# Kernel tuning notes

Hardware: AMD Instinct MI355X
Metric: run time of the kernel (lower is better)

Reference implementation:

```python
import jax, jax.numpy as jnp
import numpy as np

T = 1024
HID = 2048
N_HEADS = 32
N_KV = 8
HEAD_DIM = HID // N_HEADS  # 64
Q_SIZE = N_HEADS * HEAD_DIM
KV_SIZE = N_KV * HEAD_DIM
N_EXP = 32
TOP_K = 4
FF = 1792
EPS = 1e-5
THETA = 1e6
SCALE = HEAD_DIM ** -0.5
ROUTED_SCALE = 1.0
CAP = 2 * (T * TOP_K // N_EXP)


def rmsnorm(x, w, eps=EPS):
    xf = x.astype(jnp.float32)
    var = jnp.mean(xf * xf, axis=-1, keepdims=True)
    return ((xf * jax.lax.rsqrt(var + eps)).astype(x.dtype)) * w


def apply_rope(x, positions):
    # neox-style rotary, full head_dim. x: [T, h, D]
    half = x.shape[-1] // 2
    inv_freq = 1.0 / (THETA ** (jnp.arange(0, half, dtype=jnp.float32) / half))
    ang = positions.astype(jnp.float32)[:, None] * inv_freq  # [T, half]
    cos = jnp.cos(ang)[:, None, :]
    sin = jnp.sin(ang)[:, None, :]
    x1, x2 = x[..., :half], x[..., half:]
    return jnp.concatenate([x1 * cos - x2 * sin, x2 * cos + x1 * sin], axis=-1)


def setup_inputs() -> dict:
    key = jax.random.key(0)
    ks = jax.random.split(key, 12)
    s = 0.02
    return {
        "positions": jnp.arange(T, dtype=jnp.int32),
        "hidden_states": jax.random.normal(ks[0], (T, HID), jnp.float32),
        "residual": jax.random.normal(ks[1], (T, HID), jnp.float32),
        "w_qkv": jax.random.normal(ks[2], (HID, Q_SIZE + 2 * KV_SIZE), jnp.float32) * s,
        "w_out": jax.random.normal(ks[3], (HID, HID), jnp.float32) * s,
        "q_ln_w": 1.0 + jax.random.normal(ks[4], (HEAD_DIM,), jnp.float32) * s,
        "k_ln_w": 1.0 + jax.random.normal(ks[5], (HEAD_DIM,), jnp.float32) * s,
        "op_norm_w": 1.0 + jax.random.normal(ks[6], (HID,), jnp.float32) * s,
        "ffn_norm_w": 1.0 + jax.random.normal(ks[7], (HID,), jnp.float32) * s,
        "gate_w": jax.random.normal(ks[8], (HID, N_EXP), jnp.float32) * s,
        "gate_bias": jax.random.normal(ks[9], (N_EXP,), jnp.float32) * s,
        "w1": jax.random.normal(ks[10], (N_EXP, HID, 2 * FF), jnp.float32) * s,
        "w2": jax.random.normal(ks[11], (N_EXP, FF, HID), jnp.float32) * s,
    }


def moe_block(x, gate_w, gate_bias, w1, w2):
    # router: sigmoid scoring + correction bias for selection, weights from raw scores
    logits = (x @ gate_w).astype(jnp.float32)          # [T, E]
    scores = jax.nn.sigmoid(logits)
    _, topk_idx = jax.lax.top_k(scores + gate_bias, TOP_K)   # [T, K]
    tw = jnp.take_along_axis(scores, topk_idx, axis=-1)      # [T, K]
    tw = tw / jnp.sum(tw, axis=-1, keepdims=True)            # renormalize

    TK = T * TOP_K
    flat_e = topk_idx.reshape(-1)                      # [TK]
    flat_w = tw.reshape(-1)
    tok = jnp.repeat(jnp.arange(T), TOP_K)             # source token per pair
    order = jnp.argsort(flat_e)                        # stable group-by-expert
    se, sw, st = flat_e[order], flat_w[order], tok[order]
    counts = jnp.bincount(flat_e, length=N_EXP)
    offs = jnp.concatenate([jnp.zeros((1,), counts.dtype), jnp.cumsum(counts)[:-1]])
    pos = jnp.arange(TK) - offs[se]                    # slot within expert
    valid = (pos < CAP).astype(x.dtype)
    pos_c = jnp.minimum(pos, CAP - 1)

    # dispatch -> [E, CAP, H]
    buf = jnp.zeros((N_EXP, CAP, HID), x.dtype).at[se, pos_c].add(x[st] * valid[:, None])
    gu = jnp.einsum('ech,ehf->ecf', buf, w1)           # [E, CAP, 2F]
    g, u = gu[..., :FF], gu[..., FF:]
    h = jax.nn.silu(g) * u
    eo = jnp.einsum('ecf,efh->ech', h, w2)             # [E, CAP, H]

    # combine (gather + weighted scatter-add back to tokens)
    y_pairs = eo[se, pos_c] * (sw * valid)[:, None]
    out = jnp.zeros((T, HID), x.dtype).at[st].add(y_pairs)
    return out * ROUTED_SCALE


def reference(positions, hidden_states, residual, w_qkv, w_out, q_ln_w, k_ln_w,
              op_norm_w, ffn_norm_w, gate_w, gate_bias, w1, w2):
    # operator_norm with fused residual add
    x = hidden_states + residual
    res = x
    h = rmsnorm(x, op_norm_w)

    # attention
    qkv = h @ w_qkv
    q = qkv[:, :Q_SIZE].reshape(T, N_HEADS, HEAD_DIM)
    k = qkv[:, Q_SIZE:Q_SIZE + KV_SIZE].reshape(T, N_KV, HEAD_DIM)
    v = qkv[:, Q_SIZE + KV_SIZE:].reshape(T, N_KV, HEAD_DIM)
    q = rmsnorm(q, q_ln_w)
    k = rmsnorm(k, k_ln_w)
    q = apply_rope(q, positions)
    k = apply_rope(k, positions)
    rep = N_HEADS // N_KV
    kr = jnp.repeat(k, rep, axis=1)                    # [T, H, D]
    vr = jnp.repeat(v, rep, axis=1)
    scores = jnp.einsum('qhd,khd->hqk', q, kr) * SCALE
    causal = jnp.tril(jnp.ones((T, T), bool))
    scores = jnp.where(causal, scores, jnp.finfo(jnp.float32).min)
    p = jax.nn.softmax(scores.astype(jnp.float32), axis=-1).astype(h.dtype)
    a = jnp.einsum('hqk,khd->qhd', p, vr).reshape(T, HID)
    attn_out = a @ w_out

    # ffn_norm with fused residual add
    x2 = attn_out + res
    res2 = x2
    h2 = rmsnorm(x2, ffn_norm_w)

    out = moe_block(h2, gate_w, gate_bias, w1, w2)
    return out, res2
```

## Files before the change

### kernel.cpp

```cpp
#include <hip/hip_runtime.h>
#include <stdint.h>
#include <math.h>

typedef unsigned short ushort_t;
typedef __attribute__((ext_vector_type(8))) short short8;
typedef __attribute__((ext_vector_type(4))) float f32x4;

#define T_ 1024
#define HID_ 2048
#define NH_ 32
#define NKV_ 8
#define HD_ 64
#define QS_ 2048
#define KVS_ 512
#define QKVN_ 3072
#define NEXP_ 32
#define TOPK_ 4
#define FF_ 1792
#define FF2_ 3584
#define CAP_ 256
#define EPS_ 1e-5f
#define ATT_SCALE_ 0.125f

__device__ __forceinline__ ushort_t f2bf(float f) {
    uint32_t u = __builtin_bit_cast(uint32_t, f);
    u += 0x7FFFu + ((u >> 16) & 1u);
    return (ushort_t)(u >> 16);
}

__device__ __forceinline__ float bf2f(ushort_t u) {
    uint32_t x = ((uint32_t)u) << 16;
    return __builtin_bit_cast(float, x);
}

__device__ __forceinline__ f32x4 mfma16(short8 a, short8 b, f32x4 c) {
    return __builtin_amdgcn_mfma_f32_16x16x32_bf16(a, b, c, 0, 0, 0);
}

__device__ __forceinline__ uint32_t cvtpk(float lo, float hi) {
    uint32_t r;
    asm("v_cvt_pk_bf16_f32 %0, %1, %2" : "=v"(r) : "v"(lo), "v"(hi));
    return r;
}

__global__ __launch_bounds__(256) void k_addnorm(
    const float* __restrict__ a, const float* __restrict__ b,
    const float* __restrict__ w, float* __restrict__ res_out,
    float* __restrict__ hf, ushort_t* __restrict__ hb)
{
    __shared__ float sred[4];
    const int t = blockIdx.x;
    float x[8];
    float ss = 0.f;
#pragma unroll
    for (int i = 0; i < 8; i++) {
        int c = threadIdx.x + i * 256;
        float v = a[(size_t)t * HID_ + c];
        if (b) v += b[(size_t)t * HID_ + c];
        x[i] = v;
        ss += v * v;
    }
    ss += __shfl_xor(ss, 1);  ss += __shfl_xor(ss, 2);  ss += __shfl_xor(ss, 4);
    ss += __shfl_xor(ss, 8);  ss += __shfl_xor(ss, 16); ss += __shfl_xor(ss, 32);
    const int lane = threadIdx.x & 63, wv = threadIdx.x >> 6;
    if (lane == 0) sred[wv] = ss;
    __syncthreads();
    ss = sred[0] + sred[1] + sred[2] + sred[3];
    const float scale = rsqrtf(ss * (1.0f / HID_) + EPS_);
#pragma unroll
    for (int i = 0; i < 8; i++) {
        int c = threadIdx.x + i * 256;
        if (res_out) res_out[(size_t)t * HID_ + c] = x[i];
        float hv = x[i] * scale * w[c];
        if (hf) hf[(size_t)t * HID_ + c] = hv;
        hb[(size_t)t * HID_ + c] = f2bf(hv);
    }
}

__global__ __launch_bounds__(256) void k_rope_table(const int* __restrict__ positions,
                                                    float* __restrict__ cosb, float* __restrict__ sinb)
{
    int idx = blockIdx.x * 256 + threadIdx.x;
    if (idx >= T_ * 32) return;
    int t = idx >> 5, f = idx & 31;
    double invf = pow(1.0e6, -((double)f) / 32.0);
    double ang = (double)positions[t] * invf;
    cosb[idx] = (float)cos(ang);
    sinb[idx] = (float)sin(ang);
}

__global__ __launch_bounds__(256) void k_qkv_post(
    const float* __restrict__ qkv, const float* __restrict__ qw, const float* __restrict__ kw,
    const float* __restrict__ cosb, const float* __restrict__ sinb,
    ushort_t* __restrict__ qr, ushort_t* __restrict__ kc, ushort_t* __restrict__ vT)
{
    const int t = blockIdx.x;
    const int wv = threadIdx.x >> 6, lane = threadIdx.x & 63;
    const float* row = qkv + (size_t)t * QKVN_;
    const float c = cosb[t * 32 + (lane & 31)];
    const float s = sinb[t * 32 + (lane & 31)];
#pragma unroll
    for (int i = 0; i < 8; i++) {
        int hh = wv + i * 4;
        float x = row[hh * 64 + lane];
        float ss = x * x;
        ss += __shfl_xor(ss, 1); ss += __shfl_xor(ss, 2); ss += __shfl_xor(ss, 4);
        ss += __shfl_xor(ss, 8); ss += __shfl_xor(ss, 16); ss += __shfl_xor(ss, 32);
        float xn = x * rsqrtf(ss * (1.0f / 64.0f) + EPS_) * qw[lane];
        float other = __shfl_xor(xn, 32);
        float o = (lane < 32) ? (xn * c - other * s) : (xn * c + other * s);
        qr[(size_t)t * QS_ + hh * 64 + lane] = f2bf(o);
    }
#pragma unroll
    for (int i = 0; i < 2; i++) {
        int kh = wv * 2 + i;
        float x = row[QS_ + kh * 64 + lane];
        float ss = x * x;
        ss += __shfl_xor(ss, 1); ss += __shfl_xor(ss, 2); ss += __shfl_xor(ss, 4);
        ss += __shfl_xor(ss, 8); ss += __shfl_xor(ss, 16); ss += __shfl_xor(ss, 32);
        float xn = x * rsqrtf(ss * (1.0f / 64.0f) + EPS_) * kw[lane];
        float other = __shfl_xor(xn, 32);
        float o = (lane < 32) ? (xn * c - other * s) : (xn * c + other * s);
        kc[((size_t)kh * T_ + t) * 64 + lane] = f2bf(o);
    }
#pragma unroll
    for (int i = 0; i < 2; i++) {
        int idx = threadIdx.x + i * 256;
        int kh = idx >> 6, d = idx & 63;
        vT[((size_t)kh * 64 + d) * T_ + t] = f2bf(row[QS_ + KVS_ + idx]);
    }
}

__global__ __launch_bounds__(256) void k_attn(
    const ushort_t* __restrict__ qr, const ushort_t* __restrict__ kc,
    const ushort_t* __restrict__ vT, ushort_t* __restrict__ aout)
{
    __shared__ float p_lds[4][16][36];
    const int head = blockIdx.y;
    const int qb = blockIdx.x * 64;
    const int wv = threadIdx.x >> 6, lane = threadIdx.x & 63;
    const int lr = lane & 15, lg = lane >> 4;
    const int kvh = head >> 2;
    const int qbase = qb + wv * 16;

    const ushort_t* qp = qr + (size_t)(qbase + lr) * QS_ + head * 64 + lg * 8;
    short8 qf0 = *(const short8*)qp;
    short8 qf1 = *(const short8*)(qp + 32);

    f32x4 o[4];
#pragma unroll
    for (int i = 0; i < 4; i++) o[i] = (f32x4){0.f, 0.f, 0.f, 0.f};
    float mrow[4] = {-INFINITY, -INFINITY, -INFINITY, -INFINITY};
    float lrow[4] = {0.f, 0.f, 0.f, 0.f};

    const int ntile = ((qbase + 15) >> 5) + 1;
    for (int tt = 0; tt < ntile; tt++) {
        const int kv0 = tt * 32;
        const ushort_t* kp = kc + ((size_t)kvh * T_ + kv0) * 64;
        short8 b00 = *(const short8*)(kp + lr * 64 + lg * 8);
        short8 b01 = *(const short8*)(kp + lr * 64 + 32 + lg * 8);
        short8 b10 = *(const short8*)(kp + (16 + lr) * 64 + lg * 8);
        short8 b11 = *(const short8*)(kp + (16 + lr) * 64 + 32 + lg * 8);
        f32x4 s0 = {0.f, 0.f, 0.f, 0.f}, s1 = {0.f, 0.f, 0.f, 0.f};
        s0 = mfma16(qf0, b00, s0); s0 = mfma16(qf1, b01, s0);
        s1 = mfma16(qf0, b10, s1); s1 = mfma16(qf1, b11, s1);

        float p0[4], p1[4], alpha[4];
#pragma unroll
        for (int r = 0; r < 4; r++) {
            int qrow = qbase + lg * 4 + r;
            float v0 = (kv0 + lr <= qrow) ? s0[r] * ATT_SCALE_ : -INFINITY;
            float v1 = (kv0 + 16 + lr <= qrow) ? s1[r] * ATT_SCALE_ : -INFINITY;
            float mx = fmaxf(v0, v1);
            mx = fmaxf(mx, __shfl_xor(mx, 1));
            mx = fmaxf(mx, __shfl_xor(mx, 2));
            mx = fmaxf(mx, __shfl_xor(mx, 4));
            mx = fmaxf(mx, __shfl_xor(mx, 8));
            float mn = fmaxf(mrow[r], mx);
            float al = (mrow[r] == -INFINITY) ? 0.f : __expf(mrow[r] - mn);
            float pv0 = (v0 == -INFINITY) ? 0.f : __expf(v0 - mn);
            float pv1 = (v1 == -INFINITY) ? 0.f : __expf(v1 - mn);
            float ps = pv0 + pv1;
            ps += __shfl_xor(ps, 1); ps += __shfl_xor(ps, 2);
            ps += __shfl_xor(ps, 4); ps += __shfl_xor(ps, 8);
            lrow[r] = lrow[r] * al + ps;
            mrow[r] = mn;
            alpha[r] = al; p0[r] = pv0; p1[r] = pv1;
        }
#pragma unroll
        for (int r = 0; r < 4; r++) {
            p_lds[wv][lg * 4 + r][lr] = p0[r];
            p_lds[wv][lg * 4 + r][16 + lr] = p1[r];
            o[0][r] *= alpha[r]; o[1][r] *= alpha[r];
            o[2][r] *= alpha[r]; o[3][r] *= alpha[r];
        }
        asm volatile("s_waitcnt lgkmcnt(0)" ::: "memory");
        float4 pa0 = *(const float4*)&p_lds[wv][lr][lg * 8];
        float4 pa1 = *(const float4*)&p_lds[wv][lr][lg * 8 + 4];
        short8 pf;
        pf[0] = (short)f2bf(pa0.x); pf[1] = (short)f2bf(pa0.y);
        pf[2] = (short)f2bf(pa0.z); pf[3] = (short)f2bf(pa0.w);
        pf[4] = (short)f2bf(pa1.x); pf[5] = (short)f2bf(pa1.y);
        pf[6] = (short)f2bf(pa1.z); pf[7] = (short)f2bf(pa1.w);
#pragma unroll
        for (int dg = 0; dg < 4; dg++) {
            short8 vf = *(const short8*)(vT + ((size_t)(kvh * 64 + dg * 16 + lr)) * T_ + kv0 + lg * 8);
            o[dg] = mfma16(pf, vf, o[dg]);
        }
    }
#pragma unroll
    for (int dg = 0; dg < 4; dg++)
#pragma unroll
        for (int r = 0; r < 4; r++)
            aout[(size_t)(qbase + lg * 4 + r) * HID_ + head * 64 + dg * 16 + lr] =
                f2bf(o[dg][r] / lrow[r]);
}

template <int MODE>
__global__ __launch_bounds__(256) void k_gemm128(
    const ushort_t* __restrict__ A, const float* __restrict__ B,
    float* __restrict__ C, const float* __restrict__ resid, int N, int K, int nnb)
{
    const int nwg8 = (gridDim.x >> 3);
    const int d = blockIdx.x;
    const int wg = (d & 7) * nwg8 + (d >> 3);
    const int mbase = (wg / nnb) * 128, nbase = (wg % nnb) * 64;

    __shared__ ushort_t As[128][72];
    __shared__ ushort_t Bs[64][72];
    const int tid = threadIdx.x;
    const int lane = tid & 63, wv = tid >> 6;
    const int lr = lane & 15, lg = lane >> 4;
    const int wm = wv >> 1, wn = wv & 1;

    f32x4 acc[4][2];
#pragma unroll
    for (int i = 0; i < 4; i++)
#pragma unroll
        for (int j = 0; j < 2; j++) acc[i][j] = (f32x4){0.f, 0.f, 0.f, 0.f};

    const int arow0 = tid >> 3, achk = tid & 7;
    const int bk0 = (tid & 15) * 2, bnq = tid >> 4;
    const int bcol = nbase + bnq * 4;
    const int brow = bnq * 4;

    for (int kb = 0; kb < K; kb += 64) {
        float4 bA0 = *(const float4*)(B + (size_t)(kb + bk0) * N + bcol);
        float4 bB0 = *(const float4*)(B + (size_t)(kb + bk0 + 1) * N + bcol);
        float4 bA1 = *(const float4*)(B + (size_t)(kb + 32 + bk0) * N + bcol);
        float4 bB1 = *(const float4*)(B + (size_t)(kb + 32 + bk0 + 1) * N + bcol);
        uint4 areg[4];
#pragma unroll
        for (int i = 0; i < 4; i++)
            areg[i] = *(const uint4*)(A + (size_t)(mbase + arow0 + i * 32) * K + kb + achk * 8);
        *(uint32_t*)&Bs[brow + 0][bk0] = cvtpk(bA0.x, bB0.x);
        *(uint32_t*)&Bs[brow + 1][bk0] = cvtpk(bA0.y, bB0.y);
        *(uint32_t*)&Bs[brow + 2][bk0] = cvtpk(bA0.z, bB0.z);
        *(uint32_t*)&Bs[brow + 3][bk0] = cvtpk(bA0.w, bB0.w);
        *(uint32_t*)&Bs[brow + 0][bk0 + 32] = cvtpk(bA1.x, bB1.x);
        *(uint32_t*)&Bs[brow + 1][bk0 + 32] = cvtpk(bA1.y, bB1.y);
        *(uint32_t*)&Bs[brow + 2][bk0 + 32] = cvtpk(bA1.z, bB1.z);
        *(uint32_t*)&Bs[brow + 3][bk0 + 32] = cvtpk(bA1.w, bB1.w);
#pragma unroll
        for (int i = 0; i < 4; i++)
            *(uint4*)&As[arow0 + i * 32][achk * 8] = areg[i];
        __syncthreads();
        short8 af[4][2], bfr[2][2];
#pragma unroll
        for (int mi = 0; mi < 4; mi++)
#pragma unroll
            for (int kk = 0; kk < 2; kk++)
                af[mi][kk] = *(const short8*)&As[wm * 64 + mi * 16 + lr][kk * 32 + lg * 8];
#pragma unroll
        for (int ni = 0; ni < 2; ni++)
#pragma unroll
            for (int kk = 0; kk < 2; kk++)
                bfr[ni][kk] = *(const short8*)&Bs[wn * 32 + ni * 16 + lr][kk * 32 + lg * 8];
#pragma unroll
        for (int mi = 0; mi < 4; mi++)
#pragma unroll
            for (int ni = 0; ni < 2; ni++)
#pragma unroll
                for (int kk = 0; kk < 2; kk++)
                    acc[mi][ni] = mfma16(af[mi][kk], bfr[ni][kk], acc[mi][ni]);
        __syncthreads();
    }
#pragma unroll
    for (int mi = 0; mi < 4; mi++)
#pragma unroll
        for (int ni = 0; ni < 2; ni++)
#pragma unroll
            for (int r = 0; r < 4; r++) {
                int row = mbase + wm * 64 + mi * 16 + lg * 4 + r;
                int col = nbase + wn * 32 + ni * 16 + lr;
                float v = acc[mi][ni][r];
                if (MODE == 1) v += resid[(size_t)row * N + col];
                C[(size_t)row * N + col] = v;
            }
}

__global__ __launch_bounds__(256) void k_moe_gu(
    const ushort_t* __restrict__ h2b, const int* __restrict__ etok,
    const int* __restrict__ ecnt, const float* __restrict__ w1,
    ushort_t* __restrict__ hact)
{
    const int d = blockIdx.x;
    const int wg = (d & 7) * 224 + (d >> 3);
    const int e = wg / 56, ny = wg - e * 56;
    const int cnt = ecnt[e];
    if (cnt == 0) return;
    const int ng0 = ny * 32;
    const float* B = w1 + (size_t)e * HID_ * FF2_;

    __shared__ ushort_t As[256][72];
    __shared__ ushort_t Bs[64][72];
    const int tid = threadIdx.x;
    const int lane = tid & 63, wv = tid >> 6;
    const int lr = lane & 15, lg = lane >> 4;

    const int arow0 = tid >> 3, achk = tid & 7;
    int tok[8];
#pragma unroll
    for (int i = 0; i < 8; i++) {
        int r = arow0 + i * 32;
        tok[i] = (r < cnt) ? etok[e * CAP_ + r] : 0;
    }
    const int half = tid >> 7;
    const int t7 = tid & 127;
    const int bk0 = (t7 & 15) * 2, bnq = t7 >> 4;
    const size_t bcol = (half ? FF_ : 0) + ng0 + bnq * 4;
    const int brow = half * 32 + bnq * 4;

    f32x4 ag[4][2], au[4][2];
#pragma unroll
    for (int i = 0; i < 4; i++)
#pragma unroll
        for (int j = 0; j < 2; j++) { ag[i][j] = (f32x4){0.f,0.f,0.f,0.f}; au[i][j] = (f32x4){0.f,0.f,0.f,0.f}; }

    for (int kb = 0; kb < HID_; kb += 64) {
        float4 bA0, bB0, bA1, bB1;
        bA0 = *(const float4*)(B + (size_t)(kb + bk0) * FF2_ + bcol);
        bB0 = *(const float4*)(B + (size_t)(kb + bk0 + 1) * FF2_ + bcol);
        bA1 = *(const float4*)(B + (size_t)(kb + 32 + bk0) * FF2_ + bcol);
        bB1 = *(const float4*)(B + (size_t)(kb + 32 + bk0 + 1) * FF2_ + bcol);
        uint4 areg[8];
#pragma unroll
        for (int i = 0; i < 8; i++)
            areg[i] = *(const uint4*)(h2b + (size_t)tok[i] * HID_ + kb + achk * 8);
        *(uint32_t*)&Bs[brow + 0][bk0] = cvtpk(bA0.x, bB0.x);
        *(uint32_t*)&Bs[brow + 1][bk0] = cvtpk(bA0.y, bB0.y);
        *(uint32_t*)&Bs[brow + 2][bk0] = cvtpk(bA0.z, bB0.z);
        *(uint32_t*)&Bs[brow + 3][bk0] = cvtpk(bA0.w, bB0.w);
        *(uint32_t*)&Bs[brow + 0][bk0 + 32] = cvtpk(bA1.x, bB1.x);
        *(uint32_t*)&Bs[brow + 1][bk0 + 32] = cvtpk(bA1.y, bB1.y);
        *(uint32_t*)&Bs[brow + 2][bk0 + 32] = cvtpk(bA1.z, bB1.z);
        *(uint32_t*)&Bs[brow + 3][bk0 + 32] = cvtpk(bA1.w, bB1.w);
#pragma unroll
        for (int i = 0; i < 8; i++)
            *(uint4*)&As[arow0 + i * 32][achk * 8] = areg[i];
        __syncthreads();
        short8 af[4][2], bg[2][2], bu[2][2];
#pragma unroll
        for (int mi = 0; mi < 4; mi++)
#pragma unroll
            for (int kk = 0; kk < 2; kk++)
                af[mi][kk] = *(const short8*)&As[wv * 64 + mi * 16 + lr][kk * 32 + lg * 8];
#pragma unroll
        for (int nj = 0; nj < 2; nj++)
#pragma unroll
            for (int kk = 0; kk < 2; kk++) {
                bg[nj][kk] = *(const short8*)&Bs[nj * 16 + lr][kk * 32 + lg * 8];
                bu[nj][kk] = *(const short8*)&Bs[32 + nj * 16 + lr][kk * 32 + lg * 8];
            }
#pragma unroll
        for (int mi = 0; mi < 4; mi++)
#pragma unroll
            for (int nj = 0; nj < 2; nj++)
#pragma unroll
                for (int kk = 0; kk < 2; kk++) {
                    ag[mi][nj] = mfma16(af[mi][kk], bg[nj][kk], ag[mi][nj]);
                    au[mi][nj] = mfma16(af[mi][kk], bu[nj][kk], au[mi][nj]);
                }
        __syncthreads();
    }
#pragma unroll
    for (int mi = 0; mi < 4; mi++)
#pragma unroll
        for (int nj = 0; nj < 2; nj++)
#pragma unroll
            for (int r = 0; r < 4; r++) {
                int row = wv * 64 + mi * 16 + lg * 4 + r;
                int col = ng0 + nj * 16 + lr;
                float g = ag[mi][nj][r], u = au[mi][nj][r];
                float hval = (g / (1.0f + __expf(-g))) * u;
                hact[((size_t)e * CAP_ + row) * FF_ + col] = f2bf(hval);
            }
}

__global__ __launch_bounds__(256) void k_moe_w2(
    const ushort_t* __restrict__ hact, const float* __restrict__ w2,
    const int* __restrict__ ecnt, ushort_t* __restrict__ eo)
{
    const int d = blockIdx.x;
    const int wg = (d & 7) * 128 + (d >> 3);
    const int e = wg >> 5, nb = wg & 31;
    const int cnt = ecnt[e];
    if (cnt == 0) return;
    const int n0 = nb * 64;
    const ushort_t* A = hact + (size_t)e * CAP_ * FF_;
    const float* B = w2 + (size_t)e * FF_ * HID_;

    __shared__ ushort_t As[256][72];
    __shared__ ushort_t Bs[64][72];
    const int tid = threadIdx.x;
    const int lane = tid & 63, wv = tid >> 6;
    const int lr = lane & 15, lg = lane >> 4;

    const int arow0 = tid >> 3, achk = tid & 7;
    const int bk0 = (tid & 15) * 2, bnq = tid >> 4;
    const int bcol = n0 + bnq * 4;
    const int brow = bnq * 4;

    f32x4 acc[4][4];
#pragma unroll
    for (int i = 0; i < 4; i++)
#pragma unroll
        for (int j = 0; j < 4; j++) acc[i][j] = (f32x4){0.f, 0.f, 0.f, 0.f};

    for (int kb = 0; kb < FF_; kb += 64) {
        float4 bA0, bB0, bA1, bB1;
        bA0 = *(const float4*)(B + (size_t)(kb + bk0) * HID_ + bcol);
        bB0 = *(const float4*)(B + (size_t)(kb + bk0 + 1) * HID_ + bcol);
        bA1 = *(const float4*)(B + (size_t)(kb + 32 + bk0) * HID_ + bcol);
        bB1 = *(const float4*)(B + (size_t)(kb + 32 + bk0 + 1) * HID_ + bcol);
        uint4 areg[8];
#pragma unroll
        for (int i = 0; i < 8; i++)
            areg[i] = *(const uint4*)(A + (size_t)(arow0 + i * 32) * FF_ + kb + achk * 8);
        *(uint32_t*)&Bs[brow + 0][bk0] = cvtpk(bA0.x, bB0.x);
        *(uint32_t*)&Bs[brow + 1][bk0] = cvtpk(bA0.y, bB0.y);
        *(uint32_t*)&Bs[brow + 2][bk0] = cvtpk(bA0.z, bB0.z);
        *(uint32_t*)&Bs[brow + 3][bk0] = cvtpk(bA0.w, bB0.w);
        *(uint32_t*)&Bs[brow + 0][bk0 + 32] = cvtpk(bA1.x, bB1.x);
        *(uint32_t*)&Bs[brow + 1][bk0 + 32] = cvtpk(bA1.y, bB1.y);
        *(uint32_t*)&Bs[brow + 2][bk0 + 32] = cvtpk(bA1.z, bB1.z);
        *(uint32_t*)&Bs[brow + 3][bk0 + 32] = cvtpk(bA1.w, bB1.w);
#pragma unroll
        for (int i = 0; i < 8; i++)
            *(uint4*)&As[arow0 + i * 32][achk * 8] = areg[i];
        __syncthreads();
        short8 af[4][2], bfr[4][2];
#pragma unroll
        for (int mi = 0; mi < 4; mi++)
#pragma unroll
            for (int kk = 0; kk < 2; kk++)
                af[mi][kk] = *(const short8*)&As[wv * 64 + mi * 16 + lr][kk * 32 + lg * 8];
#pragma unroll
        for (int ni = 0; ni < 4; ni++)
#pragma unroll
            for (int kk = 0; kk < 2; kk++)
                bfr[ni][kk] = *(const short8*)&Bs[ni * 16 + lr][kk * 32 + lg * 8];
#pragma unroll
        for (int mi = 0; mi < 4; mi++)
#pragma unroll
            for (int ni = 0; ni < 4; ni++)
#pragma unroll
                for (int kk = 0; kk < 2; kk++)
                    acc[mi][ni] = mfma16(af[mi][kk], bfr[ni][kk], acc[mi][ni]);
        __syncthreads();
    }
#pragma unroll
    for (int mi = 0; mi < 4; mi++)
#pragma unroll
        for (int ni = 0; ni < 4; ni++)
#pragma unroll
            for (int r = 0; r < 4; r++) {
                int row = wv * 64 + mi * 16 + lg * 4 + r;
                int col = n0 + ni * 16 + lr;
                eo[((size_t)e * CAP_ + row) * HID_ + col] = f2bf(acc[mi][ni][r]);
            }
}

__global__ __launch_bounds__(256) void k_gate(
    const float* __restrict__ h2, const float* __restrict__ gw, const float* __restrict__ gb,
    int* __restrict__ topk_idx, float* __restrict__ topk_w)
{
    const int wv = threadIdx.x >> 6, lane = threadIdx.x & 63;
    const int t = blockIdx.x * 4 + wv;
    const float* x = h2 + (size_t)t * HID_;
    const int e = lane & 31;
    const int half = lane >> 5;
    double a0 = 0.0, a1 = 0.0, a2 = 0.0, a3 = 0.0;
    const int k0 = half * 1024;
    for (int k = 0; k < 1024; k += 4) {
        a0 += (double)x[k0 + k + 0] * (double)gw[(size_t)(k0 + k + 0) * NEXP_ + e];
        a1 += (double)x[k0 + k + 1] * (double)gw[(size_t)(k0 + k + 1) * NEXP_ + e];
        a2 += (double)x[k0 + k + 2] * (double)gw[(size_t)(k0 + k + 2) * NEXP_ + e];
        a3 += (double)x[k0 + k + 3] * (double)gw[(size_t)(k0 + k + 3) * NEXP_ + e];
    }
    double acc = (a0 + a1) + (a2 + a3);
    double other = __shfl_xor(acc, 32);
    double logit = acc + other;
    float score = (float)(1.0 / (1.0 + exp(-logit)));
    float sel = score + gb[e];

    int sel_idx[4]; float sel_w[4];
    unsigned picked = 0;
#pragma unroll
    for (int kk = 0; kk < 4; kk++) {
        float v = ((picked >> e) & 1u) ? -1e30f : sel;
        int vi = e;
#pragma unroll
        for (int m = 1; m < 32; m <<= 1) {
            float ov = __shfl_xor(v, m);
            int oi = __shfl_xor(vi, m);
            if (ov > v || (ov == v && oi < vi)) { v = ov; vi = oi; }
        }
        sel_idx[kk] = vi;
        sel_w[kk] = __shfl(score, vi);
        picked |= (1u << vi);
    }
    float wsum = sel_w[0] + sel_w[1] + sel_w[2] + sel_w[3];
    if (lane == 0) {
#pragma unroll
        for (int kk = 0; kk < 4; kk++) {
            topk_idx[t * 4 + kk] = sel_idx[kk];
            topk_w[t * 4 + kk] = sel_w[kk] / wsum;
        }
    }
}

__global__ __launch_bounds__(256) void k_route(
    const int* __restrict__ topk_idx, int* __restrict__ etok,
    int* __restrict__ ecnt, int* __restrict__ spos)
{
    const int e = blockIdx.x;
    __shared__ int wtot[4];
    __shared__ int basem;
    if (threadIdx.x == 0) basem = 0;
    __syncthreads();
    const int wv = threadIdx.x >> 6, lane = threadIdx.x & 63;
    for (int c = 0; c < 16; c++) {
        int slot = c * 256 + threadIdx.x;
        bool match = (topk_idx[slot] == e);
        unsigned long long b = __ballot(match);
        int pre = __popcll(b & ((1ull << lane) - 1ull));
        if (lane == 0) wtot[wv] = __popcll(b);
        __syncthreads();
        int off = basem;
        for (int ww = 0; ww < wv; ww++) off += wtot[ww];
        int pos = off + pre;
        if (match) {
            if (pos < CAP_) {
                etok[e * CAP_ + pos] = slot >> 2;
                spos[slot] = pos;
            } else {
                spos[slot] = -1;
            }
        }
        __syncthreads();
        if (threadIdx.x == 0) basem += wtot[0] + wtot[1] + wtot[2] + wtot[3];
        __syncthreads();
    }
    if (threadIdx.x == 0) ecnt[e] = min(basem, CAP_);
}

__global__ __launch_bounds__(256) void k_moe_out(
    const ushort_t* __restrict__ eo, const int* __restrict__ topk_idx,
    const float* __restrict__ topk_w, const int* __restrict__ spos,
    float* __restrict__ outp)
{
    const int t = blockIdx.x;
    float acc[8];
#pragma unroll
    for (int j = 0; j < 8; j++) acc[j] = 0.f;
    for (int kk = 0; kk < 4; kk++) {
        int slot = t * 4 + kk;
        int pos = spos[slot];
        if (pos < 0) continue;
        int e = topk_idx[slot];
        float wv = topk_w[slot];
        const ushort_t* er = eo + ((size_t)e * CAP_ + pos) * HID_;
#pragma unroll
        for (int j = 0; j < 8; j++) acc[j] += wv * bf2f(er[threadIdx.x + j * 256]);
    }
#pragma unroll
    for (int j = 0; j < 8; j++) outp[(size_t)t * HID_ + threadIdx.x + j * 256] = acc[j];
}

extern "C" void kernel_launch(void* const* d_in, const int* in_sizes, int n_in,
                              void* d_out, int out_size, void* d_ws, size_t ws_size,
                              hipStream_t stream)
{
    (void)in_sizes; (void)n_in; (void)out_size; (void)ws_size;
    const int* positions = (const int*)d_in[0];
    const float* hs     = (const float*)d_in[1];
    const float* residp = (const float*)d_in[2];
    const float* w_qkv  = (const float*)d_in[3];
    const float* w_out  = (const float*)d_in[4];
    const float* q_ln   = (const float*)d_in[5];
    const float* k_ln   = (const float*)d_in[6];
    const float* op_w   = (const float*)d_in[7];
    const float* ffn_w  = (const float*)d_in[8];
    const float* gate_w = (const float*)d_in[9];
    const float* gate_b = (const float*)d_in[10];
    const float* w1     = (const float*)d_in[11];
    const float* w2     = (const float*)d_in[12];

    float* outp = (float*)d_out;
    float* res2 = outp + (size_t)T_ * HID_;

    char* p = (char*)d_ws;
    auto alloc = [&](size_t bytes) -> char* {
        char* r = p;
        p += (bytes + 255) & ~(size_t)255;
        return r;
    };
    float*    res   = (float*)alloc((size_t)T_ * HID_ * 4);
    ushort_t* h     = (ushort_t*)alloc((size_t)T_ * HID_ * 2);
    float*    qkv   = (float*)alloc((size_t)T_ * QKVN_ * 4);
    ushort_t* qr    = (ushort_t*)alloc((size_t)T_ * QS_ * 2);
    ushort_t* kc    = (ushort_t*)alloc((size_t)NKV_ * T_ * HD_ * 2);
    ushort_t* vT    = (ushort_t*)alloc((size_t)NKV_ * HD_ * T_ * 2);
    ushort_t* abuf  = (ushort_t*)alloc((size_t)T_ * HID_ * 2);
    float*    h2f   = (float*)alloc((size_t)T_ * HID_ * 4);
    ushort_t* h2b   = (ushort_t*)alloc((size_t)T_ * HID_ * 2);
    float*    cosb  = (float*)alloc((size_t)T_ * 32 * 4);
    float*    sinb  = (float*)alloc((size_t)T_ * 32 * 4);
    int*      tk_i  = (int*)alloc((size_t)T_ * 4 * 4);
    float*    tk_w  = (float*)alloc((size_t)T_ * 4 * 4);
    int*      etok  = (int*)alloc((size_t)NEXP_ * CAP_ * 4);
    int*      ecnt  = (int*)alloc((size_t)NEXP_ * 4);
    int*      spos  = (int*)alloc((size_t)T_ * 4 * 4);
    ushort_t* hact  = (ushort_t*)alloc((size_t)NEXP_ * CAP_ * FF_ * 2);
    ushort_t* eo    = (ushort_t*)alloc((size_t)NEXP_ * CAP_ * HID_ * 2);

    k_addnorm<<<T_, 256, 0, stream>>>(hs, residp, op_w, res, nullptr, h);
    k_rope_table<<<(T_ * 32 + 255) / 256, 256, 0, stream>>>(positions, cosb, sinb);
    k_gemm128<0><<<(T_ / 128) * (QKVN_ / 64), 256, 0, stream>>>(
        h, w_qkv, qkv, nullptr, QKVN_, HID_, QKVN_ / 64);
    k_qkv_post<<<T_, 256, 0, stream>>>(qkv, q_ln, k_ln, cosb, sinb, qr, kc, vT);
    k_attn<<<dim3(T_ / 64, NH_), 256, 0, stream>>>(qr, kc, vT, abuf);
    k_gemm128<1><<<(T_ / 128) * (HID_ / 64), 256, 0, stream>>>(
        abuf, w_out, res2, res, HID_, HID_, HID_ / 64);
    k_addnorm<<<T_, 256, 0, stream>>>(res2, nullptr, ffn_w, nullptr, h2f, h2b);
    k_gate<<<T_ / 4, 256, 0, stream>>>(h2f, gate_w, gate_b, tk_i, tk_w);
    k_route<<<NEXP_, 256, 0, stream>>>(tk_i, etok, ecnt, spos);
    k_moe_gu<<<56 * NEXP_, 256, 0, stream>>>(h2b, etok, ecnt, w1, hact);
    k_moe_w2<<<32 * NEXP_, 256, 0, stream>>>(hact, w2, ecnt, eo);
    k_moe_out<<<T_, 256, 0, stream>>>(eo, tk_i, tk_w, spos, outp);
}
```

Baseline: 728.4 us.

## Widen attention and MoE gate/up tiles to reuse K/V and activation loads

The attention kernel now has each wave process two 16-row query strips, 64 rows apart, so every K and V fragment load serves both strips. The lower strip skips tiles beyond its causal range. The MoE gate/up kernel doubles its N tile from 32 to 64 columns, which halves the grid and the number of times gathered token rows are reloaded, at the cost of more accumulators and LDS. Both changes trade occupancy and grid parallelism for higher arithmetic intensity. The attention grid also becomes smaller and less balanced across causal rows.

Result: slower. 820.9 us (+12.7%).

```diff
diff --git a/kernel.cpp b/kernel.cpp
--- a/kernel.cpp
+++ b/kernel.cpp
@@ -137,34 +137,30 @@
 {
     __shared__ float p_lds[4][16][36];
     const int head = blockIdx.y;
-    const int qb = blockIdx.x * 64;
+    const int qb = blockIdx.x * 128;
     const int wv = threadIdx.x >> 6, lane = threadIdx.x & 63;
     const int lr = lane & 15, lg = lane >> 4;
     const int kvh = head >> 2;
-    const int qbase = qb + wv * 16;
-
-    const ushort_t* qp = qr + (size_t)(qbase + lr) * QS_ + head * 64 + lg * 8;
-    short8 qf0 = *(const short8*)qp;
-    short8 qf1 = *(const short8*)(qp + 32);
-
-    f32x4 o[4];
-#pragma unroll
-    for (int i = 0; i < 4; i++) o[i] = (f32x4){0.f, 0.f, 0.f, 0.f};
-    float mrow[4] = {-INFINITY, -INFINITY, -INFINITY, -INFINITY};
-    float lrow[4] = {0.f, 0.f, 0.f, 0.f};
-
-    const int ntile = ((qbase + 15) >> 5) + 1;
-    for (int tt = 0; tt < ntile; tt++) {
-        const int kv0 = tt * 32;
-        const ushort_t* kp = kc + ((size_t)kvh * T_ + kv0) * 64;
-        short8 b00 = *(const short8*)(kp + lr * 64 + lg * 8);
-        short8 b01 = *(const short8*)(kp + lr * 64 + 32 + lg * 8);
-        short8 b10 = *(const short8*)(kp + (16 + lr) * 64 + lg * 8);
-        short8 b11 = *(const short8*)(kp + (16 + lr) * 64 + 32 + lg * 8);
-        f32x4 s0 = {0.f, 0.f, 0.f, 0.f}, s1 = {0.f, 0.f, 0.f, 0.f};
-        s0 = mfma16(qf0, b00, s0); s0 = mfma16(qf1, b01, s0);
-        s1 = mfma16(qf0, b10, s1); s1 = mfma16(qf1, b11, s1);
-
+    const int qbase0 = qb + wv * 16;
+    const int qbase1 = qb + 64 + wv * 16;
+
+    const ushort_t* qp0 = qr + (size_t)(qbase0 + lr) * QS_ + head * 64 + lg * 8;
+    const ushort_t* qp1 = qr + (size_t)(qbase1 + lr) * QS_ + head * 64 + lg * 8;
+    short8 qa0 = *(const short8*)qp0;
+    short8 qa1 = *(const short8*)(qp0 + 32);
+    short8 qb0 = *(const short8*)qp1;
+    short8 qb1 = *(const short8*)(qp1 + 32);
+
+    f32x4 o0[4], o1[4];
+#pragma unroll
+    for (int i = 0; i < 4; i++) { o0[i] = (f32x4){0.f,0.f,0.f,0.f}; o1[i] = (f32x4){0.f,0.f,0.f,0.f}; }
+    float m0[4] = {-INFINITY,-INFINITY,-INFINITY,-INFINITY};
+    float m1[4] = {-INFINITY,-INFINITY,-INFINITY,-INFINITY};
+    float l0[4] = {0.f,0.f,0.f,0.f};
+    float l1[4] = {0.f,0.f,0.f,0.f};
+
+    auto smx = [&](f32x4 s0, f32x4 s1, int qbase, int kv0,
+                   float* mrow, float* lrow, f32x4* o) -> short8 {
         float p0[4], p1[4], alpha[4];
 #pragma unroll
         for (int r = 0; r < 4; r++) {
@@ -202,18 +198,47 @@
         pf[2] = (short)f2bf(pa0.z); pf[3] = (short)f2bf(pa0.w);
         pf[4] = (short)f2bf(pa1.x); pf[5] = (short)f2bf(pa1.y);
         pf[6] = (short)f2bf(pa1.z); pf[7] = (short)f2bf(pa1.w);
+        return pf;
+    };
+
+    const int ntile = ((qbase1 + 15) >> 5) + 1;
+    for (int tt = 0; tt < ntile; tt++) {
+        const int kv0 = tt * 32;
+        const bool act0 = (kv0 <= qbase0 + 15);
+        const ushort_t* kp = kc + ((size_t)kvh * T_ + kv0) * 64;
+        short8 b00 = *(const short8*)(kp + lr * 64 + lg * 8);
+        short8 b01 = *(const short8*)(kp + lr * 64 + 32 + lg * 8);
+        short8 b10 = *(const short8*)(kp + (16 + lr) * 64 + lg * 8);
+        short8 b11 = *(const short8*)(kp + (16 + lr) * 64 + 32 + lg * 8);
+
+        f32x4 s0 = {0.f,0.f,0.f,0.f}, s1 = {0.f,0.f,0.f,0.f};
+        s0 = mfma16(qb0, b00, s0); s0 = mfma16(qb1, b01, s0);
+        s1 = mfma16(qb0, b10, s1); s1 = mfma16(qb1, b11, s1);
+        short8 pf1 = smx(s0, s1, qbase1, kv0, m1, l1, o1);
+
+        short8 pf0;
+        if (act0) {
+            f32x4 t0 = {0.f,0.f,0.f,0.f}, t1 = {0.f,0.f,0.f,0.f};
+            t0 = mfma16(qa0, b00, t0); t0 = mfma16(qa1, b01, t0);
+            t1 = mfma16(qa0, b10, t1); t1 = mfma16(qa1, b11, t1);
+            pf0 = smx(t0, t1, qbase0, kv0, m0, l0, o0);
+        }
 #pragma unroll
         for (int dg = 0; dg < 4; dg++) {
             short8 vf = *(const short8*)(vT + ((size_t)(kvh * 64 + dg * 16 + lr)) * T_ + kv0 + lg * 8);
-            o[dg] = mfma16(pf, vf, o[dg]);
+            o1[dg] = mfma16(pf1, vf, o1[dg]);
+            if (act0) o0[dg] = mfma16(pf0, vf, o0[dg]);
         }
     }
 #pragma unroll
     for (int dg = 0; dg < 4; dg++)
 #pragma unroll
-        for (int r = 0; r < 4; r++)
-            aout[(size_t)(qbase + lg * 4 + r) * HID_ + head * 64 + dg * 16 + lr] =
-                f2bf(o[dg][r] / lrow[r]);
+        for (int r = 0; r < 4; r++) {
+            aout[(size_t)(qbase0 + lg * 4 + r) * HID_ + head * 64 + dg * 16 + lr] =
+                f2bf(o0[dg][r] / l0[r]);
+            aout[(size_t)(qbase1 + lg * 4 + r) * HID_ + head * 64 + dg * 16 + lr] =
+                f2bf(o1[dg][r] / l1[r]);
+        }
 }
 
 template <int MODE>
@@ -305,15 +330,15 @@
     ushort_t* __restrict__ hact)
 {
     const int d = blockIdx.x;
-    const int wg = (d & 7) * 224 + (d >> 3);
-    const int e = wg / 56, ny = wg - e * 56;
+    const int wg = (d & 7) * 112 + (d >> 3);
+    const int e = wg / 28, ny = wg - e * 28;
     const int cnt = ecnt[e];
     if (cnt == 0) return;
-    const int ng0 = ny * 32;
+    const int ng0 = ny * 64;
     const float* B = w1 + (size_t)e * HID_ * FF2_;
 
     __shared__ ushort_t As[256][72];
-    __shared__ ushort_t Bs[64][72];
+    __shared__ ushort_t Bs[128][72];
     const int tid = threadIdx.x;
     const int lane = tid & 63, wv = tid >> 6;
     const int lr = lane & 15, lg = lane >> 4;
@@ -328,70 +353,74 @@
     const int half = tid >> 7;
     const int t7 = tid & 127;
     const int bk0 = (t7 & 15) * 2, bnq = t7 >> 4;
-    const size_t bcol = (half ? FF_ : 0) + ng0 + bnq * 4;
-    const int brow = half * 32 + bnq * 4;
-
-    f32x4 ag[4][2], au[4][2];
+    const size_t bcolA = (half ? FF_ : 0) + ng0 + bnq * 4;
+    const size_t bcolB = bcolA + 32;
+    const int browA = half * 64 + bnq * 4;
+    const int browB = browA + 32;
+
+    f32x4 ag[4][4], au[4][4];
 #pragma unroll
     for (int i = 0; i < 4; i++)
 #pragma unroll
-        for (int j = 0; j < 2; j++) { ag[i][j] = (f32x4){0.f,0.f,0.f,0.f}; au[i][j] = (f32x4){0.f,0.f,0.f,0.f}; }
+        for (int j = 0; j < 4; j++) { ag[i][j] = (f32x4){0.f,0.f,0.f,0.f}; au[i][j] = (f32x4){0.f,0.f,0.f,0.f}; }
 
     for (int kb = 0; kb < HID_; kb += 64) {
-        float4 bA0, bB0, bA1, bB1;
-        bA0 = *(const float4*)(B + (size_t)(kb + bk0) * FF2_ + bcol);
-        bB0 = *(const float4*)(B + (size_t)(kb + bk0 + 1) * FF2_ + bcol);
-        bA1 = *(const float4*)(B + (size_t)(kb + 32 + bk0) * FF2_ + bcol);
-        bB1 = *(const float4*)(B + (size_t)(kb + 32 + bk0 + 1) * FF2_ + bcol);
-        uint4 areg[8];
-#pragma unroll
-        for (int i = 0; i < 8; i++)
-            areg[i] = *(const uint4*)(h2b + (size_t)tok[i] * HID_ + kb + achk * 8);
-        *(uint32_t*)&Bs[brow + 0][bk0] = cvtpk(bA0.x, bB0.x);
-        *(uint32_t*)&Bs[brow + 1][bk0] = cvtpk(bA0.y, bB0.y);
-        *(uint32_t*)&Bs[brow + 2][bk0] = cvtpk(bA0.z, bB0.z);
-        *(uint32_t*)&Bs[brow + 3][bk0] = cvtpk(bA0.w, bB0.w);
-        *(uint32_t*)&Bs[brow + 0][bk0 + 32] = cvtpk(bA1.x, bB1.x);
-        *(uint32_t*)&Bs[brow + 1][bk0 + 32] = cvtpk(bA1.y, bB1.y);
-        *(uint32_t*)&Bs[brow + 2][bk0 + 32] = cvtpk(bA1.z, bB1.z);
-        *(uint32_t*)&Bs[brow + 3][bk0 + 32] = cvtpk(bA1.w, bB1.w);
-#pragma unroll
-        for (int i = 0; i < 8; i++)
-            *(uint4*)&As[arow0 + i * 32][achk * 8] = areg[i];
-        __syncthreads();
-        short8 af[4][2], bg[2][2], bu[2][2];
-#pragma unroll
-        for (int mi = 0; mi < 4; mi++)
-#pragma unroll
-            for (int kk = 0; kk < 2; kk++)
-                af[mi][kk] = *(const short8*)&As[wv * 64 + mi * 16 + lr][kk * 32 + lg * 8];
-#pragma unroll
-        for (int nj = 0; nj < 2; nj++)
-#pragma unroll
-            for (int kk = 0; kk < 2; kk++) {
-                bg[nj][kk] = *(const short8*)&Bs[nj * 16 + lr][kk * 32 + lg * 8];
-                bu[nj][kk] = *(const short8*)&Bs[32 + nj * 16 + lr][kk * 32 + lg * 8];
+#pragma unroll
+        for (int ks = 0; ks < 2; ks++) {
+            const int ko = ks * 32;
+            float4 bA0 = *(const float4*)(B + (size_t)(kb + ko + bk0) * FF2_ + bcolA);
+            float4 bB0 = *(const float4*)(B + (size_t)(kb + ko + bk0 + 1) * FF2_ + bcolA);
+            float4 bA1 = *(const float4*)(B + (size_t)(kb + ko + bk0) * FF2_ + bcolB);
+            float4 bB1 = *(const float4*)(B + (size_t)(kb + ko + bk0 + 1) * FF2_ + bcolB);
+            *(uint32_t*)&Bs[browA + 0][bk0 + ko] = cvtpk(bA0.x, bB0.x);
+            *(uint32_t*)&Bs[browA + 1][bk0 + ko] = cvtpk(bA0.y, bB0.y);
+            *(uint32_t*)&Bs[browA + 2][bk0 + ko] = cvtpk(bA0.z, bB0.z);
+            *(uint32_t*)&Bs[browA + 3][bk0 + ko] = cvtpk(bA0.w, bB0.w);
+            *(uint32_t*)&Bs[browB + 0][bk0 + ko] = cvtpk(bA1.x, bB1.x);
+            *(uint32_t*)&Bs[browB + 1][bk0 + ko] = cvtpk(bA1.y, bB1.y);
+            *(uint32_t*)&Bs[browB + 2][bk0 + ko] = cvtpk(bA1.z, bB1.z);
+            *(uint32_t*)&Bs[browB + 3][bk0 + ko] = cvtpk(bA1.w, bB1.w);
+        }
+        {
+            uint4 areg[8];
+#pragma unroll
+            for (int i = 0; i < 8; i++)
+                areg[i] = *(const uint4*)(h2b + (size_t)tok[i] * HID_ + kb + achk * 8);
+#pragma unroll
+            for (int i = 0; i < 8; i++)
+                *(uint4*)&As[arow0 + i * 32][achk * 8] = areg[i];
+        }
+        __syncthreads();
+#pragma unroll
+        for (int kk = 0; kk < 2; kk++) {
+            short8 af[4], bg[4], bu[4];
+#pragma unroll
+            for (int mi = 0; mi < 4; mi++)
+                af[mi] = *(const short8*)&As[wv * 64 + mi * 16 + lr][kk * 32 + lg * 8];
+#pragma unroll
+            for (int ni = 0; ni < 4; ni++) {
+                bg[ni] = *(const short8*)&Bs[ni * 16 + lr][kk * 32 + lg * 8];
+                bu[ni] = *(const short8*)&Bs[64 + ni * 16 + lr][kk * 32 + lg * 8];
             }
 #pragma unroll
-        for (int mi = 0; mi < 4; mi++)
-#pragma unroll
-            for (int nj = 0; nj < 2; nj++)
-#pragma unroll
-                for (int kk = 0; kk < 2; kk++) {
-                    ag[mi][nj] = mfma16(af[mi][kk], bg[nj][kk], ag[mi][nj]);
-                    au[mi][nj] = mfma16(af[mi][kk], bu[nj][kk], au[mi][nj]);
+            for (int mi = 0; mi < 4; mi++)
+#pragma unroll
+                for (int ni = 0; ni < 4; ni++) {
+                    ag[mi][ni] = mfma16(af[mi], bg[ni], ag[mi][ni]);
+                    au[mi][ni] = mfma16(af[mi], bu[ni], au[mi][ni]);
                 }
+        }
         __syncthreads();
     }
 #pragma unroll
     for (int mi = 0; mi < 4; mi++)
 #pragma unroll
-        for (int nj = 0; nj < 2; nj++)
+        for (int ni = 0; ni < 4; ni++)
 #pragma unroll
             for (int r = 0; r < 4; r++) {
                 int row = wv * 64 + mi * 16 + lg * 4 + r;
-                int col = ng0 + nj * 16 + lr;
-                float g = ag[mi][nj][r], u = au[mi][nj][r];
+                int col = ng0 + ni * 16 + lr;
+                float g = ag[mi][ni][r], u = au[mi][ni][r];
                 float hval = (g / (1.0f + __expf(-g))) * u;
                 hact[((size_t)e * CAP_ + row) * FF_ + col] = f2bf(hval);
             }
@@ -640,13 +669,13 @@
     k_gemm128<0><<<(T_ / 128) * (QKVN_ / 64), 256, 0, stream>>>(
         h, w_qkv, qkv, nullptr, QKVN_, HID_, QKVN_ / 64);
     k_qkv_post<<<T_, 256, 0, stream>>>(qkv, q_ln, k_ln, cosb, sinb, qr, kc, vT);
-    k_attn<<<dim3(T_ / 64, NH_), 256, 0, stream>>>(qr, kc, vT, abuf);
+    k_attn<<<dim3(T_ / 128, NH_), 256, 0, stream>>>(qr, kc, vT, abuf);
     k_gemm128<1><<<(T_ / 128) * (HID_ / 64), 256, 0, stream>>>(
         abuf, w_out, res2, res, HID_, HID_, HID_ / 64);
     k_addnorm<<<T_, 256, 0, stream>>>(res2, nullptr, ffn_w, nullptr, h2f, h2b);
     k_gate<<<T_ / 4, 256, 0, stream>>>(h2f, gate_w, gate_b, tk_i, tk_w);
     k_route<<<NEXP_, 256, 0, stream>>>(tk_i, etok, ecnt, spos);
-    k_moe_gu<<<56 * NEXP_, 256, 0, stream>>>(h2b, etok, ecnt, w1, hact);
+    k_moe_gu<<<28 * NEXP_, 256, 0, stream>>>(h2b, etok, ecnt, w1, hact);
     k_moe_w2<<<32 * NEXP_, 256, 0, stream>>>(hact, w2, ecnt, eo);
     k_moe_out<<<T_, 256, 0, stream>>>(eo, tk_i, tk_w, spos, outp);
 }
```
